# Performance work log

Hardware: AMD Instinct MI355X
Metric: run time of the kernel (lower is better)

Reference implementation:

```python
import jax, jax.numpy as jnp
import numpy as np

B, S, D, H = 8, 1024, 1024, 16
DK = D // H  # 64


def setup_inputs() -> dict:
    key = jax.random.key(0)
    ks = jax.random.split(key, 12)
    def w(k):
        return (jax.random.normal(k, (D, D), dtype=jnp.float32) * 0.02)
    def b(k):
        return (jax.random.normal(k, (D,), dtype=jnp.float32) * 0.02)
    return {
        "q": jax.random.normal(ks[0], (B, S, D), dtype=jnp.float32),
        "k": jax.random.normal(ks[1], (B, S, D), dtype=jnp.float32),
        "v": jax.random.normal(ks[2], (B, S, D), dtype=jnp.float32),
        "mask": jax.random.randint(ks[3], (B, 1, S, S), 0, 2, dtype=jnp.int32),
        "WQ_w": w(ks[4]), "WQ_b": b(ks[5]),
        "WK_w": w(ks[6]), "WK_b": b(ks[7]),
        "WV_w": w(ks[8]), "WV_b": b(ks[9]),
        "WO_w": w(ks[10]), "WO_b": b(ks[11]),
    }


def reference(q, k, v, mask, WQ_w, WQ_b, WK_w, WK_b, WV_w, WV_b, WO_w, WO_b):
    # nn.Linear: y = x @ W.T + b
    Q = (q @ WQ_w.T + WQ_b).reshape(B, S, H, DK)
    K = (k @ WK_w.T + WK_b).reshape(B, S, H, DK)
    V = (v @ WV_w.T + WV_b).reshape(B, S, H, DK)
    # scores: [B, H, Sq, Sk]
    scores = jnp.einsum("bqhd,bkhd->bhqk", Q, K) / jnp.sqrt(jnp.float32(DK))
    scores = jnp.where(mask == 0, jnp.float32(-1e9), scores)
    attn = jax.nn.softmax(scores, axis=-1)
    # dropout p=0.0 -> identity
    out = jnp.einsum("bhqk,bkhd->bqhd", attn, V).reshape(B, S, D)
    return out @ WO_w.T + WO_b
```

## Files before the change

### kernel.cpp

```cpp
#include <hip/hip_runtime.h>
#include <math.h>

typedef __bf16 bf16;
typedef __bf16 bf16x8 __attribute__((ext_vector_type(8)));
typedef __bf16 bf16x4 __attribute__((ext_vector_type(4)));
typedef float f32x4 __attribute__((ext_vector_type(4)));

constexpr int B_ = 8, S_ = 1024, D_ = 1024, H_ = 16, DK_ = 64;
constexpr int M_ = B_ * S_;
constexpr size_t A8 = (size_t)1 << 23;
constexpr size_t W1 = (size_t)1 << 20;
constexpr float QSCALE = 0.18033688011112042f;

#if __has_builtin(__builtin_amdgcn_exp2f)
#define EXP2F(x) __builtin_amdgcn_exp2f(x)
#else
#define EXP2F(x) exp2f(x)
#endif
#if __has_builtin(__builtin_amdgcn_rcpf)
#define RCPF(x) __builtin_amdgcn_rcpf(x)
#else
#define RCPF(x) (1.0f / (x))
#endif

#define GAS(p) ((const __attribute__((address_space(1))) void*)(p))
#define LAS(p) ((__attribute__((address_space(3))) void*)(p))

template<int CTRL>
__device__ __forceinline__ float row_ror(float v) {
    int i = __builtin_bit_cast(int, v);
    i = __builtin_amdgcn_update_dpp(i, i, CTRL, 0xF, 0xF, false);
    return __builtin_bit_cast(float, i);
}
__device__ __forceinline__ float rowsum16(float v) {
    v += row_ror<0x121>(v);
    v += row_ror<0x122>(v);
    v += row_ror<0x124>(v);
    v += row_ror<0x128>(v);
    return v;
}

__global__ __launch_bounds__(256) void cvt_all(
    const float* __restrict__ q, const float* __restrict__ k,
    const float* __restrict__ v, const float* __restrict__ w0,
    const float* __restrict__ w1, const float* __restrict__ w2,
    const float* __restrict__ w3, bf16* __restrict__ dst)
{
    size_t e = ((size_t)blockIdx.x * 256 + threadIdx.x) * 8;
    const float* src;
    size_t off;
    if (e < 3 * A8) {
        int t = (int)(e >> 23);
        src = (t == 0) ? q : (t == 1) ? k : v;
        off = e & (A8 - 1);
    } else {
        size_t ew = e - 3 * A8;
        int t = (int)(ew >> 20);
        src = (t == 0) ? w0 : (t == 1) ? w1 : (t == 2) ? w2 : w3;
        off = ew & (W1 - 1);
    }
    float4 a = *(const float4*)(src + off);
    float4 b = *(const float4*)(src + off + 4);
    bf16x8 o = { (bf16)a.x, (bf16)a.y, (bf16)a.z, (bf16)a.w,
                 (bf16)b.x, (bf16)b.y, (bf16)b.z, (bf16)b.w };
    *(bf16x8*)(dst + e) = o;
}

__global__ __launch_bounds__(256) void mask_cvt(
    const int* __restrict__ mask, bf16* __restrict__ mp)
{
    const int bx = blockIdx.x;
    const int kt = bx & 15, qt = (bx >> 4) & 15, b = bx >> 8;
    const int tid = threadIdx.x;
    const int w = tid >> 6, lane = tid & 63;
    const int quad = lane >> 4, l15 = lane & 15;

    const int* src = mask + ((size_t)b << 20)
                   + (size_t)(qt * 64 + w * 16 + quad * 4) * 1024
                   + kt * 64 + l15;
    bf16 vals[16];
#pragma unroll
    for (int j = 0; j < 4; ++j)
#pragma unroll
        for (int r = 0; r < 4; ++r) {
            int m = src[(size_t)r * 1024 + j * 16];
            vals[j * 4 + r] = m ? (bf16)0.0f : (bf16)(-1e9f);
        }
    bf16* dst = mp + (((size_t)(b * 16 + qt) * 16 + kt) << 12) + (w * 64 + lane) * 16;
    bf16x8 o0 = { vals[0], vals[1], vals[2],  vals[3],  vals[4],  vals[5],  vals[6],  vals[7]  };
    bf16x8 o1 = { vals[8], vals[9], vals[10], vals[11], vals[12], vals[13], vals[14], vals[15] };
    *(bf16x8*)dst = o0;
    *(bf16x8*)(dst + 8) = o1;
}

template<int OUT_MODE>
__global__ __launch_bounds__(256) void gemm_mfma(
    const bf16* __restrict__ X, const bf16* __restrict__ W,
    const float* __restrict__ bias, void* __restrict__ outv, float oscale)
{
    constexpr int K = 1024;
    __shared__ bf16 As[128 * 32];
    __shared__ bf16 Bs[128 * 32];

    const int tid  = threadIdx.x;
    const int lane = tid & 63;
    const int w    = tid >> 6;
    const int wm   = w & 1, wn = w >> 1;
    const int quad = lane >> 4, l15 = lane & 15;
    const int bm = blockIdx.x * 128, bn = blockIdx.y * 128;

    f32x4 acc[4][4];
#pragma unroll
    for (int i = 0; i < 4; ++i)
#pragma unroll
        for (int j = 0; j < 4; ++j)
#pragma unroll
            for (int r = 0; r < 4; ++r) acc[i][j][r] = 0.f;

    const int lrow = lane >> 2;
    const int lcol = (lane & 3) * 8;

    for (int k0 = 0; k0 < K; k0 += 32) {
        __syncthreads();
#pragma unroll
        for (int i = 0; i < 2; ++i) {
            const int rbase = w * 16 + i * 64;
            __builtin_amdgcn_global_load_lds(
                GAS(X + (size_t)(bm + rbase + lrow) * K + k0 + lcol),
                LAS(As + rbase * 32), 16, 0, 0);
            __builtin_amdgcn_global_load_lds(
                GAS(W + (size_t)(bn + rbase + lrow) * K + k0 + lcol),
                LAS(Bs + rbase * 32), 16, 0, 0);
        }
        __syncthreads();

        bf16x8 a[4], b[4];
#pragma unroll
        for (int i = 0; i < 4; ++i)
            a[i] = *(const bf16x8*)(As + (wm * 64 + i * 16 + l15) * 32 + quad * 8);
#pragma unroll
        for (int j = 0; j < 4; ++j)
            b[j] = *(const bf16x8*)(Bs + (wn * 64 + j * 16 + l15) * 32 + quad * 8);
#pragma unroll
        for (int i = 0; i < 4; ++i)
#pragma unroll
            for (int j = 0; j < 4; ++j)
                acc[i][j] = __builtin_amdgcn_mfma_f32_16x16x32_bf16(
                    a[i], b[j], acc[i][j], 0, 0, 0);
    }

#pragma unroll
    for (int i = 0; i < 4; ++i) {
#pragma unroll
        for (int j = 0; j < 4; ++j) {
            const int n = bn + wn * 64 + j * 16 + l15;
            const float bs = bias[n];
            if (OUT_MODE == 2) {
                const int m0 = bm + wm * 64 + i * 16 + quad * 4;
                const int bb = m0 >> 10, s0 = m0 & 1023;
                const int h = n >> 6, dk = n & 63;
                bf16x4 o;
#pragma unroll
                for (int r = 0; r < 4; ++r) o[r] = (bf16)(acc[i][j][r] + bs);
                *(bf16x4*)((bf16*)outv + (((size_t)(bb * 16 + h) * 64 + dk) << 10) + s0) = o;
            } else {
#pragma unroll
                for (int r = 0; r < 4; ++r) {
                    const int m = bm + wm * 64 + i * 16 + quad * 4 + r;
                    const float val = acc[i][j][r] + bs;
                    if (OUT_MODE == 0) {
                        ((float*)outv)[(size_t)m * 1024 + n] = val;
                    } else {
                        const int bb = m >> 10, s = m & 1023;
                        const int h = n >> 6, dk = n & 63;
                        ((bf16*)outv)[(((size_t)(bb * 16 + h)) * 1024 + s) * 64 + dk] =
                            (bf16)(val * oscale);
                    }
                }
            }
        }
    }
}

#define LDT 72
#define PSZ (64 * 64)

__global__ __launch_bounds__(256) void attn_mfma(
    const bf16* __restrict__ Q, const bf16* __restrict__ Kt,
    const bf16* __restrict__ Vt, const bf16* __restrict__ maskp,
    bf16* __restrict__ out)
{
    __shared__ bf16 smem[2 * 64 * LDT + 4 * PSZ];
    bf16* Ks  = smem;
    bf16* Vs  = smem + 64 * LDT;
    bf16* Ps  = smem + 2 * 64 * LDT + (threadIdx.x >> 6) * PSZ;

    const int tid  = threadIdx.x;
    const int lane = tid & 63;
    const int w    = tid >> 6;
    const int quad = lane >> 4, l15 = lane & 15;

    const int q256 = blockIdx.x & 3;
    const int h    = (blockIdx.x >> 2) & 15;
    const int b    = blockIdx.x >> 6;
    const int q64  = q256 * 4 + w;

    const bf16* Qg  = Q  + ((size_t)(b * 16 + h) * 1024 + q64 * 64) * 64;
    const bf16* Kg  = Kt + ((size_t)(b * 16 + h) << 16);
    const bf16* Vgt = Vt + ((size_t)(b * 16 + h) << 16);
    const bf16* mtb = maskp + (((size_t)(b * 16 + q64) * 16) << 12) + lane * 16;

    const int rswz = ((l15 >> 2) & 3) << 4;
    const int pswz = quad << 4;

    {
        const int r8 = lane >> 3, c8 = (lane & 7) * 8;
#pragma unroll
        for (int c = 0; c < 8; ++c) {
            const int row = c * 8 + r8;
            const int key = ((row >> 2) & 3) << 4;
            *(bf16x8*)(Ps + row * 64 + (c8 ^ key)) =
                *(const bf16x8*)(Qg + row * 64 + c8);
        }
    }
    bf16x8 qa[4][2];
#pragma unroll
    for (int i = 0; i < 4; ++i)
#pragma unroll
        for (int t = 0; t < 2; ++t)
            qa[i][t] = *(const bf16x8*)(Ps + (i * 16 + l15) * 64
                                        + ((t * 32 + quad * 8) ^ rswz));

    f32x4 O[4][4];
#pragma unroll
    for (int i = 0; i < 4; ++i)
#pragma unroll
        for (int dj = 0; dj < 4; ++dj)
#pragma unroll
            for (int r = 0; r < 4; ++r) O[i][dj][r] = 0.f;
    float lrow[16];
#pragma unroll
    for (int i = 0; i < 16; ++i) lrow[i] = 0.f;

    const int rr = tid >> 3;
    const int cc = (tid & 7) * 8;

    for (int kt = 0; kt < 16; ++kt) {
        __syncthreads();
        *(bf16x8*)(Ks + rr * LDT + cc) =
            *(const bf16x8*)(Kg + kt * 4096 + rr * 64 + cc);
        *(bf16x8*)(Ks + (rr + 32) * LDT + cc) =
            *(const bf16x8*)(Kg + kt * 4096 + (rr + 32) * 64 + cc);
        *(bf16x8*)(Vs + rr * LDT + cc) =
            *(const bf16x8*)(Vgt + (size_t)rr * 1024 + kt * 64 + cc);
        *(bf16x8*)(Vs + (rr + 32) * LDT + cc) =
            *(const bf16x8*)(Vgt + (size_t)(rr + 32) * 1024 + kt * 64 + cc);
        __syncthreads();

        bf16x8 kb[2][4];
#pragma unroll
        for (int t = 0; t < 2; ++t)
#pragma unroll
            for (int j = 0; j < 4; ++j)
                kb[t][j] = *(const bf16x8*)(Ks + (j * 16 + l15) * LDT
                                            + t * 32 + quad * 8);

#pragma unroll
        for (int i = 0; i < 4; ++i) {
            f32x4 sf[4];
#pragma unroll
            for (int j = 0; j < 4; ++j)
#pragma unroll
                for (int r = 0; r < 4; ++r) sf[j][r] = 0.f;
#pragma unroll
            for (int t = 0; t < 2; ++t)
#pragma unroll
                for (int j = 0; j < 4; ++j)
                    sf[j] = __builtin_amdgcn_mfma_f32_16x16x32_bf16(
                        qa[i][t], kb[t][j], sf[j], 0, 0, 0);

            bf16x8 mv0 = *(const bf16x8*)(mtb + ((size_t)kt << 12) + (i << 10));
            bf16x8 mv1 = *(const bf16x8*)(mtb + ((size_t)kt << 12) + (i << 10) + 8);

            float psum[4] = { 0.f, 0.f, 0.f, 0.f };
#pragma unroll
            for (int j = 0; j < 4; ++j)
#pragma unroll
                for (int r = 0; r < 4; ++r) {
                    const float s = sf[j][r]
                        + (float)((j < 2 ? mv0 : mv1)[(j & 1) * 4 + r]);
                    const float p = EXP2F(s);
                    Ps[(i * 16 + quad * 4 + r) * 64 + ((j * 16 + l15) ^ pswz)]
                        = (bf16)p;
                    psum[r] += p;
                }
#pragma unroll
            for (int r = 0; r < 4; ++r)
                lrow[i * 4 + r] += rowsum16(psum[r]);
        }

#pragma unroll
        for (int t = 0; t < 2; ++t) {
            bf16x8 vb[4];
#pragma unroll
            for (int dj = 0; dj < 4; ++dj)
                vb[dj] = *(const bf16x8*)(Vs + (dj * 16 + l15) * LDT
                                          + t * 32 + quad * 8);
#pragma unroll
            for (int i = 0; i < 4; ++i) {
                bf16x8 pa = *(const bf16x8*)(Ps + (i * 16 + l15) * 64
                                             + ((t * 32 + quad * 8) ^ rswz));
#pragma unroll
                for (int dj = 0; dj < 4; ++dj)
                    O[i][dj] = __builtin_amdgcn_mfma_f32_16x16x32_bf16(
                        pa, vb[dj], O[i][dj], 0, 0, 0);
            }
        }
    }

#pragma unroll
    for (int i = 0; i < 4; ++i)
#pragma unroll
        for (int r = 0; r < 4; ++r) {
            const float rinv = RCPF(lrow[i * 4 + r]);
            const size_t row = (size_t)b * 1024 + q64 * 64 + i * 16 + quad * 4 + r;
#pragma unroll
            for (int dj = 0; dj < 4; ++dj)
                out[row * 1024 + h * 64 + dj * 16 + l15]
                    = (bf16)(O[i][dj][r] * rinv);
        }
}

extern "C" void kernel_launch(void* const* d_in, const int* in_sizes, int n_in,
                              void* d_out, int out_size, void* d_ws, size_t ws_size,
                              hipStream_t stream) {
    const float* q    = (const float*)d_in[0];
    const float* k    = (const float*)d_in[1];
    const float* v    = (const float*)d_in[2];
    const int*   mask = (const int*)d_in[3];
    const float* WQw  = (const float*)d_in[4];
    const float* WQb  = (const float*)d_in[5];
    const float* WKw  = (const float*)d_in[6];
    const float* WKb  = (const float*)d_in[7];
    const float* WVw  = (const float*)d_in[8];
    const float* WVb  = (const float*)d_in[9];
    const float* WOw  = (const float*)d_in[10];
    const float* WOb  = (const float*)d_in[11];

    bf16* ws = (bf16*)d_ws;
    bf16* qb  = ws;
    bf16* kb  = qb + A8;
    bf16* vb  = kb + A8;
    bf16* wqb = vb + A8;
    bf16* wkb = wqb + W1;
    bf16* wvb = wkb + W1;
    bf16* wob = wvb + W1;
    bf16* Qp  = wob + W1;
    bf16* Kp  = Qp + A8;
    bf16* Vp  = Kp + A8;
    bf16* maskp = qb;
    bf16* AO    = kb;

    cvt_all<<<dim3(14336), 256, 0, stream>>>(q, k, v, WQw, WKw, WVw, WOw, ws);

    dim3 gg(M_ / 128, D_ / 128);
    gemm_mfma<1><<<gg, 256, 0, stream>>>(qb, wqb, WQb, (void*)Qp, QSCALE);
    gemm_mfma<1><<<gg, 256, 0, stream>>>(kb, wkb, WKb, (void*)Kp, 1.0f);
    gemm_mfma<2><<<gg, 256, 0, stream>>>(vb, wvb, WVb, (void*)Vp, 1.0f);

    mask_cvt<<<dim3(2048), 256, 0, stream>>>(mask, maskp);

    attn_mfma<<<dim3(512), 256, 0, stream>>>(Qp, Kp, Vp, maskp, AO);

    gemm_mfma<0><<<gg, 256, 0, stream>>>(AO, wob, WOb, d_out, 1.0f);
}
```

Before: 389.9 us.

## Merge QKV projections into one launch and make attention single-wave per block

The three Q/K/V projection GEMMs now run as one launch with a z-dimension that selects input, weight, bias and output layout. The attention kernel moves from 4-wave blocks sharing LDS-staged K/V tiles to 64-thread single-wave blocks (four times as many blocks) that read Q, K and V fragments straight from global memory, keeping only the P tile in LDS. This removes the block-level barriers and K/V staging in attention and leaves fewer launches overall. The cost is that K/V reuse across the four waves now has to come from cache instead of LDS, with more global load traffic and latency exposed per wave.

After: 426.5 us. 9.4% more time.

```diff
diff --git a/kernel.cpp b/kernel.cpp
--- a/kernel.cpp
+++ b/kernel.cpp
@@ -93,32 +93,25 @@
     *(bf16x8*)(dst + 8) = o1;
 }
 
-template<int OUT_MODE>
-__global__ __launch_bounds__(256) void gemm_mfma(
+__device__ __forceinline__ void gemm_core(
     const bf16* __restrict__ X, const bf16* __restrict__ W,
-    const float* __restrict__ bias, void* __restrict__ outv, float oscale)
+    bf16* As, bf16* Bs, int bm, int bn, f32x4 (&acc)[4][4])
 {
     constexpr int K = 1024;
-    __shared__ bf16 As[128 * 32];
-    __shared__ bf16 Bs[128 * 32];
-
     const int tid  = threadIdx.x;
     const int lane = tid & 63;
     const int w    = tid >> 6;
     const int wm   = w & 1, wn = w >> 1;
     const int quad = lane >> 4, l15 = lane & 15;
-    const int bm = blockIdx.x * 128, bn = blockIdx.y * 128;
-
-    f32x4 acc[4][4];
-#pragma unroll
-    for (int i = 0; i < 4; ++i)
-#pragma unroll
-        for (int j = 0; j < 4; ++j)
-#pragma unroll
-            for (int r = 0; r < 4; ++r) acc[i][j][r] = 0.f;
-
     const int lrow = lane >> 2;
     const int lcol = (lane & 3) * 8;
+
+#pragma unroll
+    for (int i = 0; i < 4; ++i)
+#pragma unroll
+        for (int j = 0; j < 4; ++j)
+#pragma unroll
+            for (int r = 0; r < 4; ++r) acc[i][j][r] = 0.f;
 
     for (int k0 = 0; k0 < K; k0 += 32) {
         __syncthreads();
@@ -148,6 +141,34 @@
                 acc[i][j] = __builtin_amdgcn_mfma_f32_16x16x32_bf16(
                     a[i], b[j], acc[i][j], 0, 0, 0);
     }
+}
+
+__global__ __launch_bounds__(256) void gemm_qkv(
+    const bf16* __restrict__ X0, const bf16* __restrict__ X1,
+    const bf16* __restrict__ X2, const bf16* __restrict__ Wq,
+    const bf16* __restrict__ Wk, const bf16* __restrict__ Wv,
+    const float* __restrict__ bq, const float* __restrict__ bk,
+    const float* __restrict__ bv, bf16* __restrict__ oq,
+    bf16* __restrict__ ok, bf16* __restrict__ ov)
+{
+    __shared__ bf16 As[128 * 32];
+    __shared__ bf16 Bs[128 * 32];
+
+    const int z = blockIdx.z;
+    const bf16* X = (z == 0) ? X0 : (z == 1) ? X1 : X2;
+    const bf16* W = (z == 0) ? Wq : (z == 1) ? Wk : Wv;
+    const float* bias = (z == 0) ? bq : (z == 1) ? bk : bv;
+    const int bm = blockIdx.x * 128, bn = blockIdx.y * 128;
+
+    f32x4 acc[4][4];
+    gemm_core(X, W, As, Bs, bm, bn, acc);
+
+    const int tid  = threadIdx.x;
+    const int lane = tid & 63;
+    const int w    = tid >> 6;
+    const int wm   = w & 1, wn = w >> 1;
+    const int quad = lane >> 4, l15 = lane & 15;
+    const float oscale = (z == 0) ? QSCALE : 1.0f;
 
 #pragma unroll
     for (int i = 0; i < 4; ++i) {
@@ -155,81 +176,89 @@
         for (int j = 0; j < 4; ++j) {
             const int n = bn + wn * 64 + j * 16 + l15;
             const float bs = bias[n];
-            if (OUT_MODE == 2) {
+            if (z == 2) {
                 const int m0 = bm + wm * 64 + i * 16 + quad * 4;
                 const int bb = m0 >> 10, s0 = m0 & 1023;
                 const int h = n >> 6, dk = n & 63;
                 bf16x4 o;
 #pragma unroll
                 for (int r = 0; r < 4; ++r) o[r] = (bf16)(acc[i][j][r] + bs);
-                *(bf16x4*)((bf16*)outv + (((size_t)(bb * 16 + h) * 64 + dk) << 10) + s0) = o;
+                *(bf16x4*)(ov + (((size_t)(bb * 16 + h) * 64 + dk) << 10) + s0) = o;
             } else {
+                bf16* outp = (z == 0) ? oq : ok;
 #pragma unroll
                 for (int r = 0; r < 4; ++r) {
                     const int m = bm + wm * 64 + i * 16 + quad * 4 + r;
-                    const float val = acc[i][j][r] + bs;
-                    if (OUT_MODE == 0) {
-                        ((float*)outv)[(size_t)m * 1024 + n] = val;
-                    } else {
-                        const int bb = m >> 10, s = m & 1023;
-                        const int h = n >> 6, dk = n & 63;
-                        ((bf16*)outv)[(((size_t)(bb * 16 + h)) * 1024 + s) * 64 + dk] =
-                            (bf16)(val * oscale);
-                    }
+                    const int bb = m >> 10, s = m & 1023;
+                    const int h = n >> 6, dk = n & 63;
+                    outp[(((size_t)(bb * 16 + h)) * 1024 + s) * 64 + dk] =
+                        (bf16)((acc[i][j][r] + bs) * oscale);
                 }
             }
         }
     }
 }
 
-#define LDT 72
-#define PSZ (64 * 64)
-
-__global__ __launch_bounds__(256) void attn_mfma(
+__global__ __launch_bounds__(256) void gemm_o(
+    const bf16* __restrict__ X, const bf16* __restrict__ W,
+    const float* __restrict__ bias, float* __restrict__ outp)
+{
+    __shared__ bf16 As[128 * 32];
+    __shared__ bf16 Bs[128 * 32];
+    const int bm = blockIdx.x * 128, bn = blockIdx.y * 128;
+
+    f32x4 acc[4][4];
+    gemm_core(X, W, As, Bs, bm, bn, acc);
+
+    const int tid  = threadIdx.x;
+    const int lane = tid & 63;
+    const int w    = tid >> 6;
+    const int wm   = w & 1, wn = w >> 1;
+    const int quad = lane >> 4, l15 = lane & 15;
+
+#pragma unroll
+    for (int i = 0; i < 4; ++i)
+#pragma unroll
+        for (int j = 0; j < 4; ++j) {
+            const int n = bn + wn * 64 + j * 16 + l15;
+            const float bs = bias[n];
+#pragma unroll
+            for (int r = 0; r < 4; ++r) {
+                const int m = bm + wm * 64 + i * 16 + quad * 4 + r;
+                outp[(size_t)m * 1024 + n] = acc[i][j][r] + bs;
+            }
+        }
+}
+
+__global__ __launch_bounds__(64) void attn_mfma(
     const bf16* __restrict__ Q, const bf16* __restrict__ Kt,
     const bf16* __restrict__ Vt, const bf16* __restrict__ maskp,
     bf16* __restrict__ out)
 {
-    __shared__ bf16 smem[2 * 64 * LDT + 4 * PSZ];
-    bf16* Ks  = smem;
-    bf16* Vs  = smem + 64 * LDT;
-    bf16* Ps  = smem + 2 * 64 * LDT + (threadIdx.x >> 6) * PSZ;
-
-    const int tid  = threadIdx.x;
-    const int lane = tid & 63;
-    const int w    = tid >> 6;
-    const int quad = lane >> 4, l15 = lane & 15;
-
-    const int q256 = blockIdx.x & 3;
-    const int h    = (blockIdx.x >> 2) & 15;
-    const int b    = blockIdx.x >> 6;
-    const int q64  = q256 * 4 + w;
+    __shared__ bf16 Ps[64 * 64];
+
+    const int lane = threadIdx.x;
+    const int quad = lane >> 4, l15 = lane & 15;
+
+    const int q64 = blockIdx.x & 15;
+    const int h   = (blockIdx.x >> 4) & 15;
+    const int b   = blockIdx.x >> 8;
 
     const bf16* Qg  = Q  + ((size_t)(b * 16 + h) * 1024 + q64 * 64) * 64;
     const bf16* Kg  = Kt + ((size_t)(b * 16 + h) << 16);
     const bf16* Vgt = Vt + ((size_t)(b * 16 + h) << 16);
     const bf16* mtb = maskp + (((size_t)(b * 16 + q64) * 16) << 12) + lane * 16;
 
-    const int rswz = ((l15 >> 2) & 3) << 4;
     const int pswz = quad << 4;
-
-    {
-        const int r8 = lane >> 3, c8 = (lane & 7) * 8;
-#pragma unroll
-        for (int c = 0; c < 8; ++c) {
-            const int row = c * 8 + r8;
-            const int key = ((row >> 2) & 3) << 4;
-            *(bf16x8*)(Ps + row * 64 + (c8 ^ key)) =
-                *(const bf16x8*)(Qg + row * 64 + c8);
-        }
-    }
+    const int rswz = (l15 >> 2) << 4;
+
     bf16x8 qa[4][2];
 #pragma unroll
     for (int i = 0; i < 4; ++i)
 #pragma unroll
         for (int t = 0; t < 2; ++t)
-            qa[i][t] = *(const bf16x8*)(Ps + (i * 16 + l15) * 64
-                                        + ((t * 32 + quad * 8) ^ rswz));
+            qa[i][t] = *(const bf16x8*)(Qg + (size_t)(i * 16 + l15) * 64
+                                        + t * 32 + quad * 8);
 
     f32x4 O[4][4];
 #pragma unroll
@@ -242,28 +271,14 @@
 #pragma unroll
     for (int i = 0; i < 16; ++i) lrow[i] = 0.f;
 
-    const int rr = tid >> 3;
-    const int cc = (tid & 7) * 8;
-
     for (int kt = 0; kt < 16; ++kt) {
-        __syncthreads();
-        *(bf16x8*)(Ks + rr * LDT + cc) =
-            *(const bf16x8*)(Kg + kt * 4096 + rr * 64 + cc);
-        *(bf16x8*)(Ks + (rr + 32) * LDT + cc) =
-            *(const bf16x8*)(Kg + kt * 4096 + (rr + 32) * 64 + cc);
-        *(bf16x8*)(Vs + rr * LDT + cc) =
-            *(const bf16x8*)(Vgt + (size_t)rr * 1024 + kt * 64 + cc);
-        *(bf16x8*)(Vs + (rr + 32) * LDT + cc) =
-            *(const bf16x8*)(Vgt + (size_t)(rr + 32) * 1024 + kt * 64 + cc);
-        __syncthreads();
-
         bf16x8 kb[2][4];
 #pragma unroll
         for (int t = 0; t < 2; ++t)
 #pragma unroll
             for (int j = 0; j < 4; ++j)
-                kb[t][j] = *(const bf16x8*)(Ks + (j * 16 + l15) * LDT
-                                            + t * 32 + quad * 8);
+                kb[t][j] = *(const bf16x8*)(Kg
+                    + (size_t)(kt * 64 + j * 16 + l15) * 64 + t * 32 + quad * 8);
 
 #pragma unroll
         for (int i = 0; i < 4; ++i) {
@@ -304,8 +319,8 @@
             bf16x8 vb[4];
 #pragma unroll
             for (int dj = 0; dj < 4; ++dj)
-                vb[dj] = *(const bf16x8*)(Vs + (dj * 16 + l15) * LDT
-                                          + t * 32 + quad * 8);
+                vb[dj] = *(const bf16x8*)(Vgt
+                    + (size_t)(dj * 16 + l15) * 1024 + kt * 64 + t * 32 + quad * 8);
 #pragma unroll
             for (int i = 0; i < 4; ++i) {
                 bf16x8 pa = *(const bf16x8*)(Ps + (i * 16 + l15) * 64
@@ -363,14 +378,12 @@
 
     cvt_all<<<dim3(14336), 256, 0, stream>>>(q, k, v, WQw, WKw, WVw, WOw, ws);
 
-    dim3 gg(M_ / 128, D_ / 128);
-    gemm_mfma<1><<<gg, 256, 0, stream>>>(qb, wqb, WQb, (void*)Qp, QSCALE);
-    gemm_mfma<1><<<gg, 256, 0, stream>>>(kb, wkb, WKb, (void*)Kp, 1.0f);
-    gemm_mfma<2><<<gg, 256, 0, stream>>>(vb, wvb, WVb, (void*)Vp, 1.0f);
+    gemm_qkv<<<dim3(M_ / 128, D_ / 128, 3), 256, 0, stream>>>(
+        qb, kb, vb, wqb, wkb, wvb, WQb, WKb, WVb, Qp, Kp, Vp);
 
     mask_cvt<<<dim3(2048), 256, 0, stream>>>(mask, maskp);
 
-    attn_mfma<<<dim3(512), 256, 0, stream>>>(Qp, Kp, Vp, maskp, AO);
-
-    gemm_mfma<0><<<gg, 256, 0, stream>>>(AO, wob, WOb, d_out, 1.0f);
-}
+    attn_mfma<<<dim3(2048), 64, 0, stream>>>(Qp, Kp, Vp, maskp, AO);
+
+    gemm_o<<<dim3(M_ / 128, D_ / 128), 256, 0, stream>>>(AO, wob, WOb, (float*)d_out);
+}
```
